# Optimization experiments

Measured on AMD Instinct MI355X. Metric: run time of the kernel, lower is better.

The kernel has to match this reference:

```python
import jax, jax.numpy as jnp
import numpy as np

NEG_SLOPE = 0.2  # PyG GATConv default


def gat_conv(x, src, dst, W_src, W_dst, a_src, a_dst, b):
    """PyG GATConv with concat=False (mean over heads) and bias.
    x: [N, F_in]; src/dst: [E]; W_*: [F_in, H*D]; a_*: [H, D]; b: [D]."""
    N = x.shape[0]
    H, D = a_src.shape
    hs = (x @ W_src).reshape(N, H, D)
    hd = (x @ W_dst).reshape(N, H, D)
    al_s = (hs * a_src).sum(-1)  # [N, H]
    al_d = (hd * a_dst).sum(-1)  # [N, H]
    logits = jax.nn.leaky_relu(al_s[src] + al_d[dst], NEG_SLOPE)  # [E, H]
    # segment softmax over incoming edges of each dst node
    m = jax.lax.stop_gradient(jax.ops.segment_max(logits, dst, num_segments=N))
    e = jnp.exp(logits - m[dst])
    denom = jax.ops.segment_sum(e, dst, num_segments=N)  # [N, H]
    alpha = e / denom[dst]  # [E, H]
    msg = alpha[:, :, None] * hs[src]  # [E, H, D]
    out = jax.ops.segment_sum(msg, dst, num_segments=N)  # [N, H, D]
    return out.mean(axis=1) + b  # concat=False -> mean over heads


def setup_inputs() -> dict:
    key = jax.random.key(0)
    ks = jax.random.split(key, 12)
    N, F, Dh, H, E = 100000, 128, 128, 1, 1600000
    s = 0.05
    return {
        "x": jax.random.normal(ks[0], (N, F), jnp.float32),
        "edge_index": jax.random.randint(ks[1], (2, E), 0, N, jnp.int32),
        "W1_src": jax.random.normal(ks[2], (F, H * Dh), jnp.float32) * s,
        "W1_dst": jax.random.normal(ks[3], (F, H * Dh), jnp.float32) * s,
        "a1_src": jax.random.normal(ks[4], (H, Dh), jnp.float32) * s,
        "a1_dst": jax.random.normal(ks[5], (H, Dh), jnp.float32) * s,
        "b1": jnp.zeros((Dh,), jnp.float32),
        "W2_src": jax.random.normal(ks[6], (Dh, H * Dh), jnp.float32) * s,
        "W2_dst": jax.random.normal(ks[7], (Dh, H * Dh), jnp.float32) * s,
        "a2_src": jax.random.normal(ks[8], (H, Dh), jnp.float32) * s,
        "a2_dst": jax.random.normal(ks[9], (H, Dh), jnp.float32) * s,
        "b2": jnp.zeros((Dh,), jnp.float32),
    }


def reference(x, edge_index, W1_src, W1_dst, a1_src, a1_dst, b1,
              W2_src, W2_dst, a2_src, a2_dst, b2):
    src, dst = edge_index[0], edge_index[1]
    h = gat_conv(x, src, dst, W1_src, W1_dst, a1_src, a1_dst, b1)
    h = jax.nn.relu(h)  # ReLU between layers, none after the last
    out = gat_conv(h, src, dst, W2_src, W2_dst, a2_src, a2_dst, b2)
    return out
```

## Files before the change

### kernel.cpp

```cpp
#include <hip/hip_runtime.h>
#include <hip/hip_bf16.h>
#include <hip/hip_fp16.h>
#include <math.h>
#include <type_traits>


#define BKT_SHIFT 8
#define MAX_NB 512
#define EPB 2048

typedef _Float16 half8 __attribute__((ext_vector_type(8)));
typedef float floatx4 __attribute__((ext_vector_type(4)));

__global__ void prep_kernel(const float* __restrict__ W1s,
                            const float* __restrict__ a1s,
                            const float* __restrict__ W1d,
                            const float* __restrict__ a1d,
                            const float* __restrict__ W2s,
                            const float* __restrict__ a2s,
                            const float* __restrict__ W2d,
                            const float* __restrict__ a2d,
                            __half* __restrict__ wt1,
                            __half* __restrict__ wt2,
                            float* __restrict__ wv) {
    if (blockIdx.x < 32) {
        const float* W = (blockIdx.x >> 4) ? W2s : W1s;
        __half* WT = (blockIdx.x >> 4) ? wt2 : wt1;
        const int sub = blockIdx.x & 15;
        const int k0 = (sub >> 2) * 32, c0 = (sub & 3) * 32;
        __shared__ float t[32][33];
        const int r = threadIdx.x >> 5, c = threadIdx.x & 31;
        for (int rr = r; rr < 32; rr += 8)
            t[rr][c] = W[(size_t)(k0 + rr) * 128 + c0 + c];
        __syncthreads();
        for (int rr = r; rr < 32; rr += 8)
            WT[(size_t)(c0 + rr) * 128 + k0 + c] = __float2half_rn(t[c][rr]);
    } else if (threadIdx.x < 128) {
        const float* Wt[4] = {W1s, W1d, W2s, W2d};
        const float* at[4] = {a1s, a1d, a2s, a2d};
        const int b = blockIdx.x - 32;
        const float* W = Wt[b];
        const float* a = at[b];
        int k = threadIdx.x;
        float s = 0.f;
        for (int d = 0; d < 128; ++d) s += W[k * 128 + d] * a[d];
        wv[b * 128 + k] = s;
    }
}

__global__ void bucket_count_kernel(const int* __restrict__ dst,
                                    int* __restrict__ counts, int E, int NB) {
    __shared__ int h[MAX_NB];
    for (int i = threadIdx.x; i < NB; i += 256) h[i] = 0;
    __syncthreads();
    const int base = blockIdx.x * EPB;
#pragma unroll
    for (int j = 0; j < EPB / 256; ++j) {
        int i = base + j * 256 + threadIdx.x;
        if (i < E) atomicAdd(&h[dst[i] >> BKT_SHIFT], 1);
    }
    __syncthreads();
    for (int i = threadIdx.x; i < NB; i += 256)
        counts[(size_t)blockIdx.x * NB + i] = h[i];
}

__global__ void bucket_prefix_kernel(int* __restrict__ counts,
                                     int* __restrict__ totals, int NBLK,
                                     int NB) {
    __shared__ int lsum[256];
    const int b = blockIdx.x;
    const int t = threadIdx.x;
    int v[4];
    const int base = t * 4;
#pragma unroll
    for (int k = 0; k < 4; ++k) {
        int blk = base + k;
        v[k] = (blk < NBLK) ? counts[(size_t)blk * NB + b] : 0;
    }
    int s = v[0] + v[1] + v[2] + v[3];
    lsum[t] = s;
    __syncthreads();
    for (int o = 1; o < 256; o <<= 1) {
        int u = (t >= o) ? lsum[t - o] : 0;
        __syncthreads();
        lsum[t] += u;
        __syncthreads();
    }
    int run = lsum[t] - s;
#pragma unroll
    for (int k = 0; k < 4; ++k) {
        int blk = base + k;
        if (blk < NBLK) counts[(size_t)blk * NB + b] = run;
        run += v[k];
    }
    if (t == 255) totals[b] = lsum[255];
}

__global__ void bucket_base_kernel(const int* __restrict__ totals,
                                   int* __restrict__ bbase, int NB) {
    __shared__ int sh[MAX_NB];
    int t = threadIdx.x;
    int v = (t < NB) ? totals[t] : 0;
    sh[t] = v;
    __syncthreads();
    for (int o = 1; o < MAX_NB; o <<= 1) {
        int u = (t >= o) ? sh[t - o] : 0;
        __syncthreads();
        sh[t] += u;
        __syncthreads();
    }
    if (t < NB) bbase[t] = sh[t] - v;
}

__global__ void bucket_place_kernel(const int* __restrict__ src,
                                    const int* __restrict__ dst,
                                    const int* __restrict__ prefix,
                                    const int* __restrict__ bbase,
                                    int* __restrict__ bpack, int E, int NB) {
    __shared__ int cur[MAX_NB];
    const int blk = blockIdx.x;
    for (int i = threadIdx.x; i < NB; i += 256)
        cur[i] = bbase[i] + prefix[(size_t)blk * NB + i];
    __syncthreads();
    const int base = blk * EPB;
#pragma unroll
    for (int j = 0; j < EPB / 256; ++j) {
        int i = base + j * 256 + threadIdx.x;
        if (i < E) {
            int d = dst[i], s = src[i];
            int p = atomicAdd(&cur[d >> BKT_SHIFT], 1);
            bpack[p] = ((d & 255) << 17) | s;
        }
    }
}

__global__ void bucket_csr_kernel(const int* __restrict__ bpack,
                                  const int* __restrict__ bbase,
                                  int* __restrict__ row_ptr,
                                  int* __restrict__ col, int N, int E,
                                  int NB) {
    __shared__ int cnt[256];
    __shared__ int cur[256];
    const int b = blockIdx.x;
    const int t = threadIdx.x;
    const int node0 = b << BKT_SHIFT;
    const int s = bbase[b];
    const int e = (b + 1 < NB) ? bbase[b + 1] : E;
    cnt[t] = 0;
    __syncthreads();
    for (int i = s + t; i < e; i += 256) atomicAdd(&cnt[bpack[i] >> 17], 1);
    __syncthreads();
    int v = cnt[t];
    cur[t] = v;
    __syncthreads();
    for (int o = 1; o < 256; o <<= 1) {
        int u = (t >= o) ? cur[t - o] : 0;
        __syncthreads();
        cur[t] += u;
        __syncthreads();
    }
    int start = cur[t] - v;
    if (node0 + t < N) row_ptr[node0 + t] = s + start;
    __syncthreads();
    cur[t] = s + start;
    __syncthreads();
    for (int i = s + t; i < e; i += 256) {
        int pk = bpack[i];
        int p = atomicAdd(&cur[pk >> 17], 1);
        col[p] = pk & 0x1FFFF;
    }
    if (b == 0 && t == 0) row_ptr[N] = E;
}

template <typename InT>
__global__ __launch_bounds__(256) void gemm_mfma_kernel(
    const InT* __restrict__ X, const __half* __restrict__ WT,
    __half* __restrict__ C, const float* __restrict__ wvs,
    const float* __restrict__ wvd, float* __restrict__ al_s,
    float* __restrict__ al_d, int N) {
    __shared__ __align__(16) __half Ws[128][136];
    __shared__ __align__(16) __half Xs[64][136];
    const int tid = threadIdx.x;
    const int row0 = blockIdx.x * 64;

    {
        int cr = tid >> 1, off = (tid & 1) * 64;
        const __half* srcp = &WT[(size_t)cr * 128 + off];
#pragma unroll
        for (int q = 0; q < 8; ++q)
            *(float4*)&Ws[cr][off + q * 8] = *(const float4*)&srcp[q * 8];
    }
    {
        int xr = tid >> 2, co = (tid & 3) * 32;
        int gr = row0 + xr;
        if constexpr (std::is_same<InT, float>::value) {
#pragma unroll
            for (int q = 0; q < 4; ++q) {
                float4 lo = make_float4(0.f, 0.f, 0.f, 0.f);
                float4 hi = make_float4(0.f, 0.f, 0.f, 0.f);
                if (gr < N) {
                    lo = *(const float4*)&X[(size_t)gr * 128 + co + q * 8];
                    hi = *(const float4*)&X[(size_t)gr * 128 + co + q * 8 + 4];
                }
                __align__(16) __half2 tmp[4];
                tmp[0] = __floats2half2_rn(lo.x, lo.y);
                tmp[1] = __floats2half2_rn(lo.z, lo.w);
                tmp[2] = __floats2half2_rn(hi.x, hi.y);
                tmp[3] = __floats2half2_rn(hi.z, hi.w);
                *(float4*)&Xs[xr][co + q * 8] = *(const float4*)tmp;
            }
        } else {
#pragma unroll
            for (int q = 0; q < 4; ++q) {
                float4 vz = make_float4(0.f, 0.f, 0.f, 0.f);
                if (gr < N)
                    vz = *(const float4*)&X[(size_t)gr * 128 + co + q * 8];
                *(float4*)&Xs[xr][co + q * 8] = vz;
            }
        }
    }
    __syncthreads();

    const int wid = tid >> 6;
    const int lane = tid & 63;
    const int lr = lane & 15, ks = lane >> 4;
    floatx4 acc[8];
#pragma unroll
    for (int t = 0; t < 8; ++t) acc[t] = (floatx4){0.f, 0.f, 0.f, 0.f};

#pragma unroll
    for (int kk = 0; kk < 4; ++kk) {
        half8 a = *(const half8*)&Xs[wid * 16 + lr][kk * 32 + ks * 8];
#pragma unroll
        for (int t = 0; t < 8; ++t) {
            half8 b = *(const half8*)&Ws[t * 16 + lr][kk * 32 + ks * 8];
            acc[t] = __builtin_amdgcn_mfma_f32_16x16x32_f16(a, b, acc[t], 0, 0, 0);
        }
    }
#pragma unroll
    for (int r = 0; r < 4; ++r) {
        int grow = row0 + wid * 16 + ks * 4 + r;
        if (grow < N) {
#pragma unroll
            for (int t = 0; t < 8; ++t)
                C[(size_t)grow * 128 + t * 16 + lr] = __float2half_rn(acc[t][r]);
        }
    }

    {
        const int r = tid >> 2, q = tid & 3;
        float ps = 0.f, pd = 0.f;
        const int dbase = q * 32;
#pragma unroll
        for (int d = 0; d < 32; ++d) {
            float xv = __half2float(Xs[r][dbase + d]);
            ps = fmaf(xv, wvs[dbase + d], ps);
            pd = fmaf(xv, wvd[dbase + d], pd);
        }
        ps += __shfl_xor(ps, 1); ps += __shfl_xor(ps, 2);
        pd += __shfl_xor(pd, 1); pd += __shfl_xor(pd, 2);
        int gr = row0 + r;
        if (q == 0 && gr < N) { al_s[gr] = ps; al_d[gr] = pd; }
    }
}

template <typename OutT, bool RELU>
__global__ __launch_bounds__(256) void gat_aggregate_fused(
    const __half* __restrict__ hs, const float* __restrict__ al_s,
    const float* __restrict__ al_d, const int* __restrict__ row_ptr,
    const int* __restrict__ col, const float* __restrict__ bias,
    OutT* __restrict__ out, int N) {
    int node = (int)((blockIdx.x * 256u + threadIdx.x) >> 6);
    int lane = threadIdx.x & 63;
    if (node >= N) return;
    const int begin = row_ptr[node], end = row_ptr[node + 1];
    const float ald = al_d[node];
    const int d0 = lane * 2;

    float acc0 = 0.f, acc1 = 0.f, den = 0.f;
    for (int base = begin; base < end; base += 64) {
        const int cnt = min(64, end - base);
        int myidx = 0;
        float w = 0.f;
        if (lane < cnt) {
            myidx = col[base + lane];
            float l = al_s[myidx] + ald;
            l = (l >= 0.f) ? l : 0.2f * l;
            w = __expf(l);
        }
        float ws = w;
#pragma unroll
        for (int o = 32; o >= 1; o >>= 1) ws += __shfl_xor(ws, o);
        den += ws;

        for (int e = 0; e < cnt; e += 16) {
            __half2 v[16];
            float we[16];
#pragma unroll
            for (int j = 0; j < 16; ++j) {
                int s = __shfl(myidx, e + j);
                we[j] = __shfl(w, e + j);
                v[j] = *(const __half2*)&hs[((size_t)(unsigned)s << 7) + d0];
            }
#pragma unroll
            for (int j = 0; j < 16; ++j) {
                float2 f = __half22float2(v[j]);
                acc0 = fmaf(we[j], f.x, acc0);
                acc1 = fmaf(we[j], f.y, acc1);
            }
        }
    }
    const float rden = (den > 0.f) ? 1.f / den : 0.f;
    float o0 = acc0 * rden + bias[d0];
    float o1 = acc1 * rden + bias[d0 + 1];
    if (RELU) { o0 = fmaxf(o0, 0.f); o1 = fmaxf(o1, 0.f); }
    if constexpr (std::is_same<OutT, __half>::value) {
        *(__half2*)&out[(size_t)node * 128 + d0] = __floats2half2_rn(o0, o1);
    } else {
        *(float2*)&out[(size_t)node * 128 + d0] = make_float2(o0, o1);
    }
}

extern "C" void kernel_launch(void* const* d_in, const int* in_sizes, int n_in,
                              void* d_out, int out_size, void* d_ws,
                              size_t ws_size, hipStream_t stream) {
    const float* x    = (const float*)d_in[0];
    const int*  eidx  = (const int*)d_in[1];
    const float* W1s  = (const float*)d_in[2];
    const float* W1d  = (const float*)d_in[3];
    const float* a1s  = (const float*)d_in[4];
    const float* a1d  = (const float*)d_in[5];
    const float* b1   = (const float*)d_in[6];
    const float* W2s  = (const float*)d_in[7];
    const float* W2d  = (const float*)d_in[8];
    const float* a2s  = (const float*)d_in[9];
    const float* a2d  = (const float*)d_in[10];
    const float* b2   = (const float*)d_in[11];

    const int N = in_sizes[0] / 128;
    const int E = in_sizes[1] / 2;
    const int* src = eidx;
    const int* dst = eidx + E;

    const int NB   = (N + 255) >> BKT_SHIFT;
    const int NBLK = (E + EPB - 1) / EPB;

    char* p = (char*)d_ws;
    auto alloc = [&](size_t bytes) {
        char* r = p;
        p += (bytes + 255) & ~(size_t)255;
        return r;
    };
    __half* hsA   = (__half*)alloc((size_t)N * 128 * 2);
    __half* h1    = (__half*)alloc((size_t)N * 128 * 2);
    int*   row_ptr= (int*)alloc((size_t)(N + 1) * 4);
    int*   col    = (int*)alloc((size_t)E * 4);
    int*   bpack  = (int*)alloc((size_t)E * 4);
    int*   counts = (int*)alloc((size_t)NBLK * NB * 4);
    int*   totals = (int*)alloc(MAX_NB * 4);
    int*   bbase  = (int*)alloc(MAX_NB * 4);
    float* al_s   = (float*)alloc((size_t)N * 4);
    float* al_d   = (float*)alloc((size_t)N * 4);
    float* wv     = (float*)alloc(4 * 128 * 4);
    __half* wt1   = (__half*)alloc(128 * 128 * 2);
    __half* wt2   = (__half*)alloc(128 * 128 * 2);

    prep_kernel<<<36, 256, 0, stream>>>(W1s, a1s, W1d, a1d, W2s, a2s, W2d,
                                        a2d, wt1, wt2, wv);

    bucket_count_kernel<<<NBLK, 256, 0, stream>>>(dst, counts, E, NB);
    bucket_prefix_kernel<<<NB, 256, 0, stream>>>(counts, totals, NBLK, NB);
    bucket_base_kernel<<<1, MAX_NB, 0, stream>>>(totals, bbase, NB);
    bucket_place_kernel<<<NBLK, 256, 0, stream>>>(src, dst, counts, bbase,
                                                  bpack, E, NB);
    bucket_csr_kernel<<<NB, 256, 0, stream>>>(bpack, bbase, row_ptr, col, N, E,
                                              NB);

    const int gemm_grid = (N + 63) / 64;
    const int wave_grid = (N + 3) / 4;

    gemm_mfma_kernel<float><<<gemm_grid, 256, 0, stream>>>(
        x, wt1, hsA, wv + 0, wv + 128, al_s, al_d, N);
    gat_aggregate_fused<__half, true><<<wave_grid, 256, 0, stream>>>(
        hsA, al_s, al_d, row_ptr, col, b1, h1, N);

    gemm_mfma_kernel<__half><<<gemm_grid, 256, 0, stream>>>(
        h1, wt2, hsA, wv + 256, wv + 384, al_s, al_d, N);
    gat_aggregate_fused<float, false><<<wave_grid, 256, 0, stream>>>(
        hsA, al_s, al_d, row_ptr, col, b2, (float*)d_out, N);
}
```

Before: 245.7 us.

## Fuse CSR construction and weight prep into one cooperative kernel with grid syncs

Replaces the six launches (weight prep, bucket count, prefix, base scan, place, per-bucket CSR) with a single cooperative kernel that runs each phase and separates them with grid.sync(). The aim is to remove per-launch overhead and idle gaps between the small, dependent kernels. The trade-off is that all NBLK+36 blocks (about 818) must be co-resident for the cooperative launch, and grid-wide barriers cost something, while later phases use only NB blocks. The final base scan also changes from a 512-thread block to 256 threads handling two elements each.

```diff
diff --git a/kernel.cpp b/kernel.cpp
--- a/kernel.cpp
+++ b/kernel.cpp
@@ -1,9 +1,12 @@
 #include <hip/hip_runtime.h>
+#include <hip/hip_cooperative_groups.h>
 #include <hip/hip_bf16.h>
 #include <hip/hip_fp16.h>
 #include <math.h>
 #include <type_traits>
 
+namespace cg = cooperative_groups;
+
 
 #define BKT_SHIFT 8
 #define MAX_NB 512
@@ -12,164 +15,154 @@
 typedef _Float16 half8 __attribute__((ext_vector_type(8)));
 typedef float floatx4 __attribute__((ext_vector_type(4)));
 
-__global__ void prep_kernel(const float* __restrict__ W1s,
-                            const float* __restrict__ a1s,
-                            const float* __restrict__ W1d,
-                            const float* __restrict__ a1d,
-                            const float* __restrict__ W2s,
-                            const float* __restrict__ a2s,
-                            const float* __restrict__ W2d,
-                            const float* __restrict__ a2d,
-                            __half* __restrict__ wt1,
-                            __half* __restrict__ wt2,
-                            float* __restrict__ wv) {
-    if (blockIdx.x < 32) {
-        const float* W = (blockIdx.x >> 4) ? W2s : W1s;
-        __half* WT = (blockIdx.x >> 4) ? wt2 : wt1;
-        const int sub = blockIdx.x & 15;
+__global__ __launch_bounds__(256) void csr_coop_kernel(
+    const int* __restrict__ src, const int* __restrict__ dst,
+    const float* __restrict__ W1s, const float* __restrict__ a1s,
+    const float* __restrict__ W1d, const float* __restrict__ a1d,
+    const float* __restrict__ W2s, const float* __restrict__ a2s,
+    const float* __restrict__ W2d, const float* __restrict__ a2d,
+    __half* __restrict__ wt1, __half* __restrict__ wt2,
+    float* __restrict__ wv, int* __restrict__ counts,
+    int* __restrict__ totals, int* __restrict__ bbase,
+    int* __restrict__ bpack, int* __restrict__ row_ptr,
+    int* __restrict__ col, int N, int E, int NB, int NBLK) {
+    cg::grid_group grid = cg::this_grid();
+    __shared__ int sA[MAX_NB];
+    __shared__ int sB[256];
+    __shared__ float wtile[32][33];
+    const int bid = blockIdx.x;
+    const int t = threadIdx.x;
+
+    if (bid < NBLK) {
+        for (int i = t; i < NB; i += 256) sA[i] = 0;
+        __syncthreads();
+        const int base = bid * EPB;
+#pragma unroll
+        for (int j = 0; j < EPB / 256; ++j) {
+            int i = base + j * 256 + t;
+            if (i < E) atomicAdd(&sA[dst[i] >> BKT_SHIFT], 1);
+        }
+        __syncthreads();
+        for (int i = t; i < NB; i += 256)
+            counts[(size_t)bid * NB + i] = sA[i];
+    } else if (bid < NBLK + 32) {
+        const int wb = bid - NBLK;
+        const float* W = (wb >> 4) ? W2s : W1s;
+        __half* WT = (wb >> 4) ? wt2 : wt1;
+        const int sub = wb & 15;
         const int k0 = (sub >> 2) * 32, c0 = (sub & 3) * 32;
-        __shared__ float t[32][33];
-        const int r = threadIdx.x >> 5, c = threadIdx.x & 31;
+        const int r = t >> 5, c = t & 31;
         for (int rr = r; rr < 32; rr += 8)
-            t[rr][c] = W[(size_t)(k0 + rr) * 128 + c0 + c];
+            wtile[rr][c] = W[(size_t)(k0 + rr) * 128 + c0 + c];
         __syncthreads();
         for (int rr = r; rr < 32; rr += 8)
-            WT[(size_t)(c0 + rr) * 128 + k0 + c] = __float2half_rn(t[c][rr]);
-    } else if (threadIdx.x < 128) {
-        const float* Wt[4] = {W1s, W1d, W2s, W2d};
-        const float* at[4] = {a1s, a1d, a2s, a2d};
-        const int b = blockIdx.x - 32;
-        const float* W = Wt[b];
-        const float* a = at[b];
-        int k = threadIdx.x;
-        float s = 0.f;
-        for (int d = 0; d < 128; ++d) s += W[k * 128 + d] * a[d];
-        wv[b * 128 + k] = s;
-    }
-}
-
-__global__ void bucket_count_kernel(const int* __restrict__ dst,
-                                    int* __restrict__ counts, int E, int NB) {
-    __shared__ int h[MAX_NB];
-    for (int i = threadIdx.x; i < NB; i += 256) h[i] = 0;
-    __syncthreads();
-    const int base = blockIdx.x * EPB;
-#pragma unroll
-    for (int j = 0; j < EPB / 256; ++j) {
-        int i = base + j * 256 + threadIdx.x;
-        if (i < E) atomicAdd(&h[dst[i] >> BKT_SHIFT], 1);
-    }
-    __syncthreads();
-    for (int i = threadIdx.x; i < NB; i += 256)
-        counts[(size_t)blockIdx.x * NB + i] = h[i];
-}
-
-__global__ void bucket_prefix_kernel(int* __restrict__ counts,
-                                     int* __restrict__ totals, int NBLK,
-                                     int NB) {
-    __shared__ int lsum[256];
-    const int b = blockIdx.x;
-    const int t = threadIdx.x;
-    int v[4];
-    const int base = t * 4;
-#pragma unroll
-    for (int k = 0; k < 4; ++k) {
-        int blk = base + k;
-        v[k] = (blk < NBLK) ? counts[(size_t)blk * NB + b] : 0;
-    }
-    int s = v[0] + v[1] + v[2] + v[3];
-    lsum[t] = s;
-    __syncthreads();
-    for (int o = 1; o < 256; o <<= 1) {
-        int u = (t >= o) ? lsum[t - o] : 0;
-        __syncthreads();
-        lsum[t] += u;
-        __syncthreads();
-    }
-    int run = lsum[t] - s;
-#pragma unroll
-    for (int k = 0; k < 4; ++k) {
-        int blk = base + k;
-        if (blk < NBLK) counts[(size_t)blk * NB + b] = run;
-        run += v[k];
-    }
-    if (t == 255) totals[b] = lsum[255];
-}
-
-__global__ void bucket_base_kernel(const int* __restrict__ totals,
-                                   int* __restrict__ bbase, int NB) {
-    __shared__ int sh[MAX_NB];
-    int t = threadIdx.x;
-    int v = (t < NB) ? totals[t] : 0;
-    sh[t] = v;
-    __syncthreads();
-    for (int o = 1; o < MAX_NB; o <<= 1) {
-        int u = (t >= o) ? sh[t - o] : 0;
-        __syncthreads();
-        sh[t] += u;
-        __syncthreads();
-    }
-    if (t < NB) bbase[t] = sh[t] - v;
-}
-
-__global__ void bucket_place_kernel(const int* __restrict__ src,
-                                    const int* __restrict__ dst,
-                                    const int* __restrict__ prefix,
-                                    const int* __restrict__ bbase,
-                                    int* __restrict__ bpack, int E, int NB) {
-    __shared__ int cur[MAX_NB];
-    const int blk = blockIdx.x;
-    for (int i = threadIdx.x; i < NB; i += 256)
-        cur[i] = bbase[i] + prefix[(size_t)blk * NB + i];
-    __syncthreads();
-    const int base = blk * EPB;
-#pragma unroll
-    for (int j = 0; j < EPB / 256; ++j) {
-        int i = base + j * 256 + threadIdx.x;
-        if (i < E) {
-            int d = dst[i], s = src[i];
-            int p = atomicAdd(&cur[d >> BKT_SHIFT], 1);
-            bpack[p] = ((d & 255) << 17) | s;
-        }
-    }
-}
-
-__global__ void bucket_csr_kernel(const int* __restrict__ bpack,
-                                  const int* __restrict__ bbase,
-                                  int* __restrict__ row_ptr,
-                                  int* __restrict__ col, int N, int E,
-                                  int NB) {
-    __shared__ int cnt[256];
-    __shared__ int cur[256];
-    const int b = blockIdx.x;
-    const int t = threadIdx.x;
-    const int node0 = b << BKT_SHIFT;
-    const int s = bbase[b];
-    const int e = (b + 1 < NB) ? bbase[b + 1] : E;
-    cnt[t] = 0;
-    __syncthreads();
-    for (int i = s + t; i < e; i += 256) atomicAdd(&cnt[bpack[i] >> 17], 1);
-    __syncthreads();
-    int v = cnt[t];
-    cur[t] = v;
-    __syncthreads();
-    for (int o = 1; o < 256; o <<= 1) {
-        int u = (t >= o) ? cur[t - o] : 0;
-        __syncthreads();
-        cur[t] += u;
-        __syncthreads();
-    }
-    int start = cur[t] - v;
-    if (node0 + t < N) row_ptr[node0 + t] = s + start;
-    __syncthreads();
-    cur[t] = s + start;
-    __syncthreads();
-    for (int i = s + t; i < e; i += 256) {
-        int pk = bpack[i];
-        int p = atomicAdd(&cur[pk >> 17], 1);
-        col[p] = pk & 0x1FFFF;
-    }
-    if (b == 0 && t == 0) row_ptr[N] = E;
+            WT[(size_t)(c0 + rr) * 128 + k0 + c] = __float2half_rn(wtile[c][rr]);
+    } else if (bid < NBLK + 36) {
+        if (t < 128) {
+            const float* Wt[4] = {W1s, W1d, W2s, W2d};
+            const float* at[4] = {a1s, a1d, a2s, a2d};
+            const int b = bid - NBLK - 32;
+            const float* W = Wt[b];
+            const float* a = at[b];
+            float s = 0.f;
+            for (int d = 0; d < 128; ++d) s += W[t * 128 + d] * a[d];
+            wv[b * 128 + t] = s;
+        }
+    }
+    grid.sync();
+
+    if (bid < NB) {
+        int v[4];
+        const int base = t * 4;
+#pragma unroll
+        for (int k = 0; k < 4; ++k) {
+            int blk = base + k;
+            v[k] = (blk < NBLK) ? counts[(size_t)blk * NB + bid] : 0;
+        }
+        int s = v[0] + v[1] + v[2] + v[3];
+        sA[t] = s;
+        __syncthreads();
+        for (int o = 1; o < 256; o <<= 1) {
+            int u = (t >= o) ? sA[t - o] : 0;
+            __syncthreads();
+            sA[t] += u;
+            __syncthreads();
+        }
+        int run = sA[t] - s;
+#pragma unroll
+        for (int k = 0; k < 4; ++k) {
+            int blk = base + k;
+            if (blk < NBLK) counts[(size_t)blk * NB + bid] = run;
+            run += v[k];
+        }
+        if (t == 255) totals[bid] = sA[255];
+    }
+    grid.sync();
+
+    if (bid == 0) {
+        int v0 = (2 * t < NB) ? totals[2 * t] : 0;
+        int v1 = (2 * t + 1 < NB) ? totals[2 * t + 1] : 0;
+        int s = v0 + v1;
+        sA[t] = s;
+        __syncthreads();
+        for (int o = 1; o < 256; o <<= 1) {
+            int u = (t >= o) ? sA[t - o] : 0;
+            __syncthreads();
+            sA[t] += u;
+            __syncthreads();
+        }
+        int excl = sA[t] - s;
+        if (2 * t < NB) bbase[2 * t] = excl;
+        if (2 * t + 1 < NB) bbase[2 * t + 1] = excl + v0;
+    }
+    grid.sync();
+
+    if (bid < NBLK) {
+        for (int i = t; i < NB; i += 256)
+            sA[i] = bbase[i] + counts[(size_t)bid * NB + i];
+        __syncthreads();
+        const int base = bid * EPB;
+#pragma unroll
+        for (int j = 0; j < EPB / 256; ++j) {
+            int i = base + j * 256 + t;
+            if (i < E) {
+                int d = dst[i], s = src[i];
+                int p = atomicAdd(&sA[d >> BKT_SHIFT], 1);
+                bpack[p] = ((d & 255) << 17) | s;
+            }
+        }
+    }
+    grid.sync();
+
+    if (bid < NB) {
+        const int node0 = bid << BKT_SHIFT;
+        const int s = bbase[bid];
+        const int e = (bid + 1 < NB) ? bbase[bid + 1] : E;
+        sA[t] = 0;
+        __syncthreads();
+        for (int i = s + t; i < e; i += 256) atomicAdd(&sA[bpack[i] >> 17], 1);
+        __syncthreads();
+        int v = sA[t];
+        sB[t] = v;
+        __syncthreads();
+        for (int o = 1; o < 256; o <<= 1) {
+            int u = (t >= o) ? sB[t - o] : 0;
+            __syncthreads();
+            sB[t] += u;
+            __syncthreads();
+        }
+        int start = sB[t] - v;
+        if (node0 + t < N) row_ptr[node0 + t] = s + start;
+        __syncthreads();
+        sB[t] = s + start;
+        __syncthreads();
+        for (int i = s + t; i < e; i += 256) {
+            int pk = bpack[i];
+            int p = atomicAdd(&sB[pk >> 17], 1);
+            col[p] = pk & 0x1FFFF;
+        }
+        if (bid == 0 && t == 0) row_ptr[N] = E;
+    }
 }
 
 template <typename InT>
@@ -337,13 +330,13 @@
     const float* a2d  = (const float*)d_in[10];
     const float* b2   = (const float*)d_in[11];
 
-    const int N = in_sizes[0] / 128;
-    const int E = in_sizes[1] / 2;
+    int N = in_sizes[0] / 128;
+    int E = in_sizes[1] / 2;
     const int* src = eidx;
     const int* dst = eidx + E;
 
-    const int NB   = (N + 255) >> BKT_SHIFT;
-    const int NBLK = (E + EPB - 1) / EPB;
+    int NB   = (N + 255) >> BKT_SHIFT;
+    int NBLK = (E + EPB - 1) / EPB;
 
     char* p = (char*)d_ws;
     auto alloc = [&](size_t bytes) {
@@ -365,16 +358,18 @@
     __half* wt1   = (__half*)alloc(128 * 128 * 2);
     __half* wt2   = (__half*)alloc(128 * 128 * 2);
 
-    prep_kernel<<<36, 256, 0, stream>>>(W1s, a1s, W1d, a1d, W2s, a2s, W2d,
-                                        a2d, wt1, wt2, wv);
-
-    bucket_count_kernel<<<NBLK, 256, 0, stream>>>(dst, counts, E, NB);
-    bucket_prefix_kernel<<<NB, 256, 0, stream>>>(counts, totals, NBLK, NB);
-    bucket_base_kernel<<<1, MAX_NB, 0, stream>>>(totals, bbase, NB);
-    bucket_place_kernel<<<NBLK, 256, 0, stream>>>(src, dst, counts, bbase,
-                                                  bpack, E, NB);
-    bucket_csr_kernel<<<NB, 256, 0, stream>>>(bpack, bbase, row_ptr, col, N, E,
-                                              NB);
+    {
+        void* args[] = {(void*)&src,  (void*)&dst,  (void*)&W1s, (void*)&a1s,
+                        (void*)&W1d,  (void*)&a1d,  (void*)&W2s, (void*)&a2s,
+                        (void*)&W2d,  (void*)&a2d,  (void*)&wt1, (void*)&wt2,
+                        (void*)&wv,   (void*)&counts, (void*)&totals,
+                        (void*)&bbase, (void*)&bpack, (void*)&row_ptr,
+                        (void*)&col,  (void*)&N,    (void*)&E,   (void*)&NB,
+                        (void*)&NBLK};
+        hipLaunchCooperativeKernel((const void*)csr_coop_kernel,
+                                   dim3(NBLK + 36), dim3(256), args, 0,
+                                   stream);
+    }
 
     const int gemm_grid = (N + 63) / 64;
     const int wave_grid = (N + 3) / 4;
```

Result: slower. 642.2 us (+161.4%).

## Replace per-block bucket prefix scan with global atomic bucket cursors

Applied to the files above, without the earlier changes.

Removes the per-block counts matrix and its column-prefix kernel. Histogram blocks now atomically add into global bucket totals, and the weight prep work is merged into the same launch. The place kernel builds a local histogram, reserves ranges via atomics on global cursors, then scatters. This cuts one kernel launch and the counts traffic, at the cost of a memset, global atomics and a non-deterministic edge order within buckets.

```diff
diff --git a/kernel.cpp b/kernel.cpp
--- a/kernel.cpp
+++ b/kernel.cpp
@@ -12,92 +12,59 @@
 typedef _Float16 half8 __attribute__((ext_vector_type(8)));
 typedef float floatx4 __attribute__((ext_vector_type(4)));
 
-__global__ void prep_kernel(const float* __restrict__ W1s,
-                            const float* __restrict__ a1s,
-                            const float* __restrict__ W1d,
-                            const float* __restrict__ a1d,
-                            const float* __restrict__ W2s,
-                            const float* __restrict__ a2s,
-                            const float* __restrict__ W2d,
-                            const float* __restrict__ a2d,
-                            __half* __restrict__ wt1,
-                            __half* __restrict__ wt2,
-                            float* __restrict__ wv) {
-    if (blockIdx.x < 32) {
-        const float* W = (blockIdx.x >> 4) ? W2s : W1s;
-        __half* WT = (blockIdx.x >> 4) ? wt2 : wt1;
-        const int sub = blockIdx.x & 15;
+__global__ __launch_bounds__(256) void bucket_hist_prep_kernel(
+    const int* __restrict__ dst, int* __restrict__ totals,
+    const float* __restrict__ W1s, const float* __restrict__ a1s,
+    const float* __restrict__ W1d, const float* __restrict__ a1d,
+    const float* __restrict__ W2s, const float* __restrict__ a2s,
+    const float* __restrict__ W2d, const float* __restrict__ a2d,
+    __half* __restrict__ wt1, __half* __restrict__ wt2,
+    float* __restrict__ wv, int E, int NB, int NBLK) {
+    const int bid = blockIdx.x;
+    const int t = threadIdx.x;
+    if (bid < NBLK) {
+        __shared__ int h[MAX_NB];
+        for (int i = t; i < NB; i += 256) h[i] = 0;
+        __syncthreads();
+        const int base = bid * EPB;
+#pragma unroll
+        for (int j = 0; j < EPB / 256; ++j) {
+            int i = base + j * 256 + t;
+            if (i < E) atomicAdd(&h[dst[i] >> BKT_SHIFT], 1);
+        }
+        __syncthreads();
+        for (int i = t; i < NB; i += 256)
+            if (h[i] > 0) atomicAdd(&totals[i], h[i]);
+    } else if (bid < NBLK + 32) {
+        __shared__ float wtile[32][33];
+        const int wb = bid - NBLK;
+        const float* W = (wb >> 4) ? W2s : W1s;
+        __half* WT = (wb >> 4) ? wt2 : wt1;
+        const int sub = wb & 15;
         const int k0 = (sub >> 2) * 32, c0 = (sub & 3) * 32;
-        __shared__ float t[32][33];
-        const int r = threadIdx.x >> 5, c = threadIdx.x & 31;
+        const int r = t >> 5, c = t & 31;
         for (int rr = r; rr < 32; rr += 8)
-            t[rr][c] = W[(size_t)(k0 + rr) * 128 + c0 + c];
+            wtile[rr][c] = W[(size_t)(k0 + rr) * 128 + c0 + c];
         __syncthreads();
         for (int rr = r; rr < 32; rr += 8)
-            WT[(size_t)(c0 + rr) * 128 + k0 + c] = __float2half_rn(t[c][rr]);
-    } else if (threadIdx.x < 128) {
-        const float* Wt[4] = {W1s, W1d, W2s, W2d};
-        const float* at[4] = {a1s, a1d, a2s, a2d};
-        const int b = blockIdx.x - 32;
-        const float* W = Wt[b];
-        const float* a = at[b];
-        int k = threadIdx.x;
-        float s = 0.f;
-        for (int d = 0; d < 128; ++d) s += W[k * 128 + d] * a[d];
-        wv[b * 128 + k] = s;
-    }
-}
-
-__global__ void bucket_count_kernel(const int* __restrict__ dst,
-                                    int* __restrict__ counts, int E, int NB) {
-    __shared__ int h[MAX_NB];
-    for (int i = threadIdx.x; i < NB; i += 256) h[i] = 0;
-    __syncthreads();
-    const int base = blockIdx.x * EPB;
-#pragma unroll
-    for (int j = 0; j < EPB / 256; ++j) {
-        int i = base + j * 256 + threadIdx.x;
-        if (i < E) atomicAdd(&h[dst[i] >> BKT_SHIFT], 1);
-    }
-    __syncthreads();
-    for (int i = threadIdx.x; i < NB; i += 256)
-        counts[(size_t)blockIdx.x * NB + i] = h[i];
-}
-
-__global__ void bucket_prefix_kernel(int* __restrict__ counts,
-                                     int* __restrict__ totals, int NBLK,
-                                     int NB) {
-    __shared__ int lsum[256];
-    const int b = blockIdx.x;
-    const int t = threadIdx.x;
-    int v[4];
-    const int base = t * 4;
-#pragma unroll
-    for (int k = 0; k < 4; ++k) {
-        int blk = base + k;
-        v[k] = (blk < NBLK) ? counts[(size_t)blk * NB + b] : 0;
-    }
-    int s = v[0] + v[1] + v[2] + v[3];
-    lsum[t] = s;
-    __syncthreads();
-    for (int o = 1; o < 256; o <<= 1) {
-        int u = (t >= o) ? lsum[t - o] : 0;
-        __syncthreads();
-        lsum[t] += u;
-        __syncthreads();
-    }
-    int run = lsum[t] - s;
-#pragma unroll
-    for (int k = 0; k < 4; ++k) {
-        int blk = base + k;
-        if (blk < NBLK) counts[(size_t)blk * NB + b] = run;
-        run += v[k];
-    }
-    if (t == 255) totals[b] = lsum[255];
+            WT[(size_t)(c0 + rr) * 128 + k0 + c] = __float2half_rn(wtile[c][rr]);
+    } else {
+        if (t < 128) {
+            const float* Wt[4] = {W1s, W1d, W2s, W2d};
+            const float* at[4] = {a1s, a1d, a2s, a2d};
+            const int b = bid - NBLK - 32;
+            const float* W = Wt[b];
+            const float* a = at[b];
+            float s = 0.f;
+            for (int d = 0; d < 128; ++d) s += W[t * 128 + d] * a[d];
+            wv[b * 128 + t] = s;
+        }
+    }
 }
 
 __global__ void bucket_base_kernel(const int* __restrict__ totals,
-                                   int* __restrict__ bbase, int NB) {
+                                   int* __restrict__ bbase,
+                                   int* __restrict__ gcur, int NB) {
     __shared__ int sh[MAX_NB];
     int t = threadIdx.x;
     int v = (t < NB) ? totals[t] : 0;
@@ -109,27 +76,45 @@
         sh[t] += u;
         __syncthreads();
     }
-    if (t < NB) bbase[t] = sh[t] - v;
-}
-
-__global__ void bucket_place_kernel(const int* __restrict__ src,
-                                    const int* __restrict__ dst,
-                                    const int* __restrict__ prefix,
-                                    const int* __restrict__ bbase,
-                                    int* __restrict__ bpack, int E, int NB) {
-    __shared__ int cur[MAX_NB];
-    const int blk = blockIdx.x;
-    for (int i = threadIdx.x; i < NB; i += 256)
-        cur[i] = bbase[i] + prefix[(size_t)blk * NB + i];
-    __syncthreads();
-    const int base = blk * EPB;
-#pragma unroll
-    for (int j = 0; j < EPB / 256; ++j) {
-        int i = base + j * 256 + threadIdx.x;
-        if (i < E) {
-            int d = dst[i], s = src[i];
-            int p = atomicAdd(&cur[d >> BKT_SHIFT], 1);
-            bpack[p] = ((d & 255) << 17) | s;
+    if (t < NB) {
+        int excl = sh[t] - v;
+        bbase[t] = excl;
+        gcur[t] = excl;
+    }
+}
+
+__global__ __launch_bounds__(256) void bucket_place_kernel(
+    const int* __restrict__ src, const int* __restrict__ dst,
+    int* __restrict__ gcur, int* __restrict__ bpack, int E, int NB) {
+    __shared__ int h[MAX_NB];
+    const int bid = blockIdx.x;
+    const int t = threadIdx.x;
+    const int base = bid * EPB;
+    int d[8], s[8];
+    bool ok[8];
+#pragma unroll
+    for (int j = 0; j < 8; ++j) {
+        int i = base + j * 256 + t;
+        ok[j] = (i < E);
+        d[j] = ok[j] ? dst[i] : 0;
+        s[j] = ok[j] ? src[i] : 0;
+    }
+    for (int i = t; i < NB; i += 256) h[i] = 0;
+    __syncthreads();
+#pragma unroll
+    for (int j = 0; j < 8; ++j)
+        if (ok[j]) atomicAdd(&h[d[j] >> BKT_SHIFT], 1);
+    __syncthreads();
+    for (int i = t; i < NB; i += 256) {
+        int c = h[i];
+        if (c > 0) h[i] = atomicAdd(&gcur[i], c);
+    }
+    __syncthreads();
+#pragma unroll
+    for (int j = 0; j < 8; ++j) {
+        if (ok[j]) {
+            int p = atomicAdd(&h[d[j] >> BKT_SHIFT], 1);
+            bpack[p] = ((d[j] & 255) << 17) | s[j];
         }
     }
 }
@@ -356,23 +341,22 @@
     int*   row_ptr= (int*)alloc((size_t)(N + 1) * 4);
     int*   col    = (int*)alloc((size_t)E * 4);
     int*   bpack  = (int*)alloc((size_t)E * 4);
-    int*   counts = (int*)alloc((size_t)NBLK * NB * 4);
     int*   totals = (int*)alloc(MAX_NB * 4);
     int*   bbase  = (int*)alloc(MAX_NB * 4);
+    int*   gcur   = (int*)alloc(MAX_NB * 4);
     float* al_s   = (float*)alloc((size_t)N * 4);
     float* al_d   = (float*)alloc((size_t)N * 4);
     float* wv     = (float*)alloc(4 * 128 * 4);
     __half* wt1   = (__half*)alloc(128 * 128 * 2);
     __half* wt2   = (__half*)alloc(128 * 128 * 2);
 
-    prep_kernel<<<36, 256, 0, stream>>>(W1s, a1s, W1d, a1d, W2s, a2s, W2d,
-                                        a2d, wt1, wt2, wv);
-
-    bucket_count_kernel<<<NBLK, 256, 0, stream>>>(dst, counts, E, NB);
-    bucket_prefix_kernel<<<NB, 256, 0, stream>>>(counts, totals, NBLK, NB);
-    bucket_base_kernel<<<1, MAX_NB, 0, stream>>>(totals, bbase, NB);
-    bucket_place_kernel<<<NBLK, 256, 0, stream>>>(src, dst, counts, bbase,
-                                                  bpack, E, NB);
+    hipMemsetAsync(totals, 0, (size_t)NB * 4, stream);
+    bucket_hist_prep_kernel<<<NBLK + 36, 256, 0, stream>>>(
+        dst, totals, W1s, a1s, W1d, a1d, W2s, a2s, W2d, a2d, wt1, wt2, wv, E,
+        NB, NBLK);
+    bucket_base_kernel<<<1, MAX_NB, 0, stream>>>(totals, bbase, gcur, NB);
+    bucket_place_kernel<<<NBLK, 256, 0, stream>>>(src, dst, gcur, bpack, E,
+                                                  NB);
     bucket_csr_kernel<<<NB, 256, 0, stream>>>(bpack, bbase, row_ptr, col, N, E,
                                               NB);
 
```

Result: slower. 266.1 us (+8.3%).
